# Performance work log

Measured on AMD Instinct MI355X. Metric: run time of the kernel, lower is better.

Reference implementation:

```python
import jax, jax.numpy as jnp
import numpy as np

B, N, K, D, H = 8, 128, 64, 256, 8  # batch, groups, keys-per-query, k_dim (=h_size), n_head


def setup_inputs() -> dict:
    key = jax.random.key(0)
    kq, kk, kv, kw, kb = jax.random.split(key, 5)
    bound = 1.0 / np.sqrt(D)  # torch nn.Bilinear default init bound
    return {
        "q": jax.random.normal(kq, (B, N, 1, D), jnp.float32),
        "k": jax.random.normal(kk, (B, N, K, D), jnp.float32),
        "v": jax.random.normal(kv, (B, N, K, D), jnp.float32),
        "W": jax.random.uniform(kw, (H, D, D), jnp.float32, -bound, bound),
        "b": jax.random.uniform(kb, (H,), jnp.float32, -bound, bound),
    }


def reference(q, k, v, W, b):
    Bs, Ns, Ks, Ds = k.shape
    Hh = W.shape[0]
    qe = q[:, :, 0, :]  # (B,N,D); torch expands q over K, einsum broadcasts instead
    # nn.Bilinear: scores[b,n,k,h] = q[b,n,:] @ W[h] @ k[b,n,k,:] + b[h]
    scores = jnp.einsum('bnd,hde,bnke->bnkh', qe, W, k) + b  # (B,N,K,H)
    # Faithful to torch's .view(B, N, -1, K): row-major reinterpretation of the
    # trailing (K, H) pair as (H, K) — a dim-mixing reshape, not a transpose.
    attn = scores.reshape(Bs, Ns, Hh, Ks)
    attn = jax.nn.softmax(attn, axis=-1)  # softmax over last dim (dropout p=0)
    # matmul(attn, v) -> (B,N,H,Dv); then sum over the head axis
    output = jnp.einsum('bnhk,bnkd->bnd', attn, v)
    return output, attn
```

## Files before the change

kernel.cpp:

```cpp
#include <hip/hip_runtime.h>
#include <math.h>

namespace {

constexpr int D = 256;
constexpr int H = 8;

typedef __attribute__((ext_vector_type(8))) short bf16x8;
typedef __attribute__((ext_vector_type(4))) float f32x4;

__device__ inline unsigned short bf16rn(float x) {
  unsigned u = __builtin_bit_cast(unsigned, x);
  u += 0x7fffu + ((u >> 16) & 1u);
  return (unsigned short)(u >> 16);
}
__device__ inline float bf16tof(unsigned short b) {
  return __builtin_bit_cast(float, (unsigned)b << 16);
}

constexpr size_t OFF_QW  = 0;
constexpr size_t OFF_WFH = (size_t)8 << 20;
constexpr size_t OFF_WFL = (size_t)9 << 20;
constexpr size_t OFF_QFH = (size_t)10 << 20;
constexpr size_t OFF_QFL = ((size_t)10 << 20) + ((size_t)512 << 10);

__global__ __launch_bounds__(256) void prep_kernel(
    const float* __restrict__ q, const float* __restrict__ W,
    char* __restrict__ ws) {
  const int gid = blockIdx.x * 256 + threadIdx.x;
  float e[8];
  char *hi_base, *lo_base;
  size_t outoff;
  if (gid < 65536) {
    const int l = gid & 63, ks = (gid >> 6) & 7, he = gid >> 9;
    const int h = he >> 4, et = he & 15;
    const int d0 = ks * 32 + ((l >> 4) << 3);
    const int ecol = et * 16 + (l & 15);
    const float* src = W + (size_t)h * 65536 + (size_t)d0 * 256 + ecol;
    #pragma unroll
    for (int j = 0; j < 8; ++j) e[j] = src[j * 256];
    hi_base = ws + OFF_WFH; lo_base = ws + OFF_WFL;
    outoff = (size_t)gid * 16;
  } else {
    const int t = gid - 65536;
    const int l = t & 63, ks = (t >> 6) & 7, bt = t >> 9;
    const int row = bt * 16 + (l & 15);
    const int d0 = ks * 32 + ((l >> 4) << 3);
    const float4* src = reinterpret_cast<const float4*>(q + (size_t)row * 256 + d0);
    float4 a = src[0], b = src[1];
    e[0] = a.x; e[1] = a.y; e[2] = a.z; e[3] = a.w;
    e[4] = b.x; e[5] = b.y; e[6] = b.z; e[7] = b.w;
    hi_base = ws + OFF_QFH; lo_base = ws + OFF_QFL;
    outoff = (size_t)t * 16;
  }
  unsigned hw[4], lw[4];
  #pragma unroll
  for (int p = 0; p < 4; ++p) {
    unsigned short h0 = bf16rn(e[2 * p]), h1 = bf16rn(e[2 * p + 1]);
    unsigned short l0 = bf16rn(e[2 * p] - bf16tof(h0));
    unsigned short l1 = bf16rn(e[2 * p + 1] - bf16tof(h1));
    hw[p] = (unsigned)h0 | ((unsigned)h1 << 16);
    lw[p] = (unsigned)l0 | ((unsigned)l1 << 16);
  }
  *reinterpret_cast<uint4*>(hi_base + outoff) = make_uint4(hw[0], hw[1], hw[2], hw[3]);
  *reinterpret_cast<uint4*>(lo_base + outoff) = make_uint4(lw[0], lw[1], lw[2], lw[3]);
}

__global__ __launch_bounds__(256) void qw_mfma_kernel(
    const char* __restrict__ ws_in, float* __restrict__ qW) {
  const int tid = threadIdx.x;
  const int w   = blockIdx.x * 4 + (tid >> 6);
  const int l   = tid & 63;
  const int bng = w >> 5;
  const int heg = w & 31;
  const char* qfh = ws_in + OFF_QFH;
  const char* qfl = ws_in + OFF_QFL;
  const char* wfh = ws_in + OFF_WFH;
  const char* wfl = ws_in + OFF_WFL;

  f32x4 acc[2][4];
  #pragma unroll
  for (int i = 0; i < 2; ++i)
    #pragma unroll
    for (int j = 0; j < 4; ++j) acc[i][j] = {0.f, 0.f, 0.f, 0.f};

  #pragma unroll 2
  for (int ks = 0; ks < 8; ++ks) {
    bf16x8 aH[2], aL[2], bH[4], bL[4];
    #pragma unroll
    for (int i = 0; i < 2; ++i) {
      const size_t off = ((size_t)((bng * 2 + i) * 8 + ks) * 64 + l) * 16;
      aH[i] = *reinterpret_cast<const bf16x8*>(qfh + off);
      aL[i] = *reinterpret_cast<const bf16x8*>(qfl + off);
    }
    #pragma unroll
    for (int j = 0; j < 4; ++j) {
      const size_t off = ((size_t)((heg * 4 + j) * 8 + ks) * 64 + l) * 16;
      bH[j] = *reinterpret_cast<const bf16x8*>(wfh + off);
      bL[j] = *reinterpret_cast<const bf16x8*>(wfl + off);
    }
    #pragma unroll
    for (int i = 0; i < 2; ++i)
      #pragma unroll
      for (int j = 0; j < 4; ++j) {
        acc[i][j] = __builtin_amdgcn_mfma_f32_16x16x32_bf16(aH[i], bH[j], acc[i][j], 0, 0, 0);
        acc[i][j] = __builtin_amdgcn_mfma_f32_16x16x32_bf16(aH[i], bL[j], acc[i][j], 0, 0, 0);
        acc[i][j] = __builtin_amdgcn_mfma_f32_16x16x32_bf16(aL[i], bH[j], acc[i][j], 0, 0, 0);
      }
  }

  const int rbase = (l >> 4) * 4;
  const int col   = l & 15;
  #pragma unroll
  for (int i = 0; i < 2; ++i)
    #pragma unroll
    for (int j = 0; j < 4; ++j) {
      const size_t cidx = (size_t)(heg * 4 + j) * 16 + col;
      #pragma unroll
      for (int r = 0; r < 4; ++r) {
        const int bn = (bng * 2 + i) * 16 + rbase + r;
        qW[(size_t)bn * 2048 + cidx] = acc[i][j][r];
      }
    }
}

constexpr int FA_HI = 0;
constexpr int FB_HI = 16640;
constexpr int WSP_OFF = 24960;
constexpr int SMEM2 = 25472;

__global__ __launch_bounds__(256, 4) void attn_fused_kernel(
    const float* __restrict__ qW, const float* __restrict__ kin,
    const float* __restrict__ vin, const float* __restrict__ bin,
    float* __restrict__ out, float* __restrict__ attn_out) {
  __shared__ alignas(16) long long smem_ll[SMEM2 / 8];
  char* sm = reinterpret_cast<char*>(smem_ll);
  float* wsp = reinterpret_cast<float*>(sm + WSP_OFF);
  const int tid = threadIdx.x;
  const int bn  = blockIdx.x;
  const int wid = tid >> 6;
  const int ln  = tid & 63;

  const float4* k4  = reinterpret_cast<const float4*>(kin) + (size_t)bn * 4096;
  const float4* v4  = reinterpret_cast<const float4*>(vin) + (size_t)bn * 4096;
  const float4* qw4 = reinterpret_cast<const float4*>(qW) + (size_t)bn * 512;
  const float bias = bin[ln & 7];

  float4 kv1[8];
  #pragma unroll
  for (int i = 0; i < 8; ++i) kv1[i] = k4[tid + 256 * i];
  float4 qv0 = qw4[tid];
  float4 qv1 = qw4[tid + 256];

  {
    const int ks = tid >> 5, slot = 32 + (tid & 31);
    *reinterpret_cast<uint4*>(sm + FB_HI + ks * 1040 + slot * 16) =
        make_uint4(0u, 0u, 0u, 0u);
  }

  auto convert_k = [&](const float4* kv) {
    #pragma unroll
    for (int i = 0; i < 8; ++i) {
      int quad = tid + 256 * i;
      int row = quad >> 6, equad = quad & 63;
      int tile = row >> 4, lrow = row & 15;
      int ks = equad >> 3, g = (equad >> 1) & 3, j0 = (equad & 1) * 4;
      int base = tile * 8320 + ks * 1040 + (lrow * 4 + g) * 16 + j0 * 2;
      unsigned short h0 = bf16rn(kv[i].x), h1 = bf16rn(kv[i].y),
                     h2 = bf16rn(kv[i].z), h3 = bf16rn(kv[i].w);
      uint2 hw = make_uint2((unsigned)h0 | ((unsigned)h1 << 16),
                            (unsigned)h2 | ((unsigned)h3 << 16));
      *reinterpret_cast<uint2*>(sm + FA_HI + base) = hw;
    }
  };

  convert_k(kv1);
  #pragma unroll
  for (int i = 0; i < 2; ++i) {
    int p = tid + 256 * i;
    int hh = p >> 6, equad = p & 63;
    int ks = equad >> 3, g = (equad >> 1) & 3, j0 = (equad & 1) * 4;
    int base = ks * 1040 + (hh * 4 + g) * 16 + j0 * 2;
    float4 qv = i == 0 ? qv0 : qv1;
    unsigned short h0 = bf16rn(qv.x), h1 = bf16rn(qv.y),
                   h2 = bf16rn(qv.z), h3 = bf16rn(qv.w);
    uint2 hw = make_uint2((unsigned)h0 | ((unsigned)h1 << 16),
                          (unsigned)h2 | ((unsigned)h3 << 16));
    *reinterpret_cast<uint2*>(sm + FB_HI + base) = hw;
  }

  float4 kv2[8];
  #pragma unroll
  for (int i = 0; i < 8; ++i) kv2[i] = k4[2048 + tid + 256 * i];
  __builtin_amdgcn_sched_barrier(0);
  __syncthreads();

  auto do_phase = [&](int kh, bool first) {
    const int T = wid;
    const int slot_r = (ln & 15) * 4 + (ln >> 4);
    const char* paH = sm + FA_HI + T * 8320 + slot_r * 16;
    const char* pbH = sm + FB_HI + slot_r * 16;
    f32x4 acc = {0.f, 0.f, 0.f, 0.f};
    #pragma unroll
    for (int ks = 0; ks < 8; ++ks) {
      bf16x8 aH = *reinterpret_cast<const bf16x8*>(paH + ks * 1040);
      bf16x8 bH = *reinterpret_cast<const bf16x8*>(pbH + ks * 1040);
      acc = __builtin_amdgcn_mfma_f32_16x16x32_bf16(aH, bH, acc, 0, 0, 0);
    }
    const int col = ln & 15;
    const bool valid = col < 8;
    float x0 = acc[0] + bias, x1 = acc[1] + bias, x2 = acc[2] + bias, x3 = acc[3] + bias;
    float m = valid ? fmaxf(fmaxf(x0, x1), fmaxf(x2, x3)) : -1e30f;
    m = fmaxf(m, __shfl_xor(m, 1, 64));
    m = fmaxf(m, __shfl_xor(m, 2, 64));
    m = fmaxf(m, __shfl_xor(m, 4, 64));
    m = fmaxf(m, __shfl_xor(m, 16, 64));
    float e0 = valid ? expf(x0 - m) : 0.f;
    float e1 = valid ? expf(x1 - m) : 0.f;
    float e2 = valid ? expf(x2 - m) : 0.f;
    float e3 = valid ? expf(x3 - m) : 0.f;
    float s = e0 + e1 + e2 + e3;
    s += __shfl_xor(s, 1, 64);
    s += __shfl_xor(s, 2, 64);
    s += __shfl_xor(s, 4, 64);
    s += __shfl_xor(s, 16, 64);
    float inv = 1.f / s;
    float p0 = e0 * inv, p1 = e1 * inv, p2 = e2 * inv, p3 = e3 * inv;
    if (valid) {
      size_t base = (size_t)bn * 512 + (size_t)(kh * 32 + T * 16 + (ln >> 4) * 4) * 8 + col;
      attn_out[base]      = p0;
      attn_out[base + 8]  = p1;
      attn_out[base + 16] = p2;
      attn_out[base + 24] = p3;
    }
    p0 += __shfl_xor(p0, 32, 64);
    p1 += __shfl_xor(p1, 32, 64);
    p2 += __shfl_xor(p2, 32, 64);
    p3 += __shfl_xor(p3, 32, 64);
    if (ln < 32 && (ln & 15) < 8) {
      const int rb = (ln >> 4) * 4;
      const int c8 = ln & 7;
      float* w = wsp + T * 64;
      if (first) {
        w[(rb + 0) * 8 + c8] = p0;
        w[(rb + 1) * 8 + c8] = p1;
        w[(rb + 2) * 8 + c8] = p2;
        w[(rb + 3) * 8 + c8] = p3;
      } else {
        w[(rb + 0) * 8 + c8] += p0;
        w[(rb + 1) * 8 + c8] += p1;
        w[(rb + 2) * 8 + c8] += p2;
        w[(rb + 3) * 8 + c8] += p3;
      }
    }
  };

  if (wid < 2) do_phase(0, true);
  __syncthreads();

  convert_k(kv2);
  float4 vv[16];
  #pragma unroll
  for (int i = 0; i < 16; ++i) vv[i] = v4[(wid + 4 * i) * 64 + ln];
  __builtin_amdgcn_sched_barrier(0);
  __syncthreads();

  if (wid < 2) do_phase(1, false);
  __syncthreads();

  float4 acc = make_float4(0.f, 0.f, 0.f, 0.f);
  #pragma unroll
  for (int i = 0; i < 16; ++i) {
    const int r = wid + 4 * i;
    float w = wsp[r] + wsp[64 + r];
    acc.x += w * vv[i].x; acc.y += w * vv[i].y;
    acc.z += w * vv[i].z; acc.w += w * vv[i].w;
  }
  float* s_red = reinterpret_cast<float*>(sm);
  *reinterpret_cast<float4*>(&s_red[wid * 260 + (ln << 2)]) = acc;
  __syncthreads();

  out[(size_t)bn * D + tid] =
      s_red[tid] + s_red[260 + tid] + s_red[520 + tid] + s_red[780 + tid];
}

}

extern "C" void kernel_launch(void* const* d_in, const int* in_sizes, int n_in,
                              void* d_out, int out_size, void* d_ws, size_t ws_size,
                              hipStream_t stream) {
  const float* q = (const float*)d_in[0];
  const float* k = (const float*)d_in[1];
  const float* v = (const float*)d_in[2];
  const float* W = (const float*)d_in[3];
  const float* b = (const float*)d_in[4];

  float* out  = (float*)d_out;
  float* attn = out + 262144;
  char*  ws   = (char*)d_ws;
  float* qWbuf = (float*)(ws + OFF_QW);

  hipLaunchKernelGGL(prep_kernel,       dim3(384),  dim3(256), 0, stream, q, W, ws);
  hipLaunchKernelGGL(qw_mfma_kernel,    dim3(256),  dim3(256), 0, stream, ws, qWbuf);
  hipLaunchKernelGGL(attn_fused_kernel, dim3(1024), dim3(256), 0, stream,
                     qWbuf, k, v, b, out, attn);
}
```

Measured before the change: 43.53 us.

## Load K directly into MFMA registers and use all four waves for scores

Each wave now loads its 16 K rows from global memory straight into registers in MFMA A-operand layout and converts them to bf16 in registers, which removes the LDS staging of K and its two-phase schedule. All four waves compute scores and softmax in one pass instead of two waves over two phases, and per-wave weights are summed in the V reduction. V loads move after the softmax barrier and are issued inline, so they no longer overlap the score computation. LDS use drops substantially, which may allow higher occupancy, but global K loads are now strided per lane.

```diff
diff --git a/kernel.cpp b/kernel.cpp
--- a/kernel.cpp
+++ b/kernel.cpp
@@ -124,160 +124,122 @@
     }
 }
 
-constexpr int FA_HI = 0;
-constexpr int FB_HI = 16640;
-constexpr int WSP_OFF = 24960;
-constexpr int SMEM2 = 25472;
+constexpr int FB2   = 0;
+constexpr int WSP2  = 8320;
+constexpr int SMEM3 = 9344;
 
 __global__ __launch_bounds__(256, 4) void attn_fused_kernel(
     const float* __restrict__ qW, const float* __restrict__ kin,
     const float* __restrict__ vin, const float* __restrict__ bin,
     float* __restrict__ out, float* __restrict__ attn_out) {
-  __shared__ alignas(16) long long smem_ll[SMEM2 / 8];
+  __shared__ alignas(16) long long smem_ll[SMEM3 / 8];
   char* sm = reinterpret_cast<char*>(smem_ll);
-  float* wsp = reinterpret_cast<float*>(sm + WSP_OFF);
+  float* wsp = reinterpret_cast<float*>(sm + WSP2);
   const int tid = threadIdx.x;
   const int bn  = blockIdx.x;
   const int wid = tid >> 6;
   const int ln  = tid & 63;
 
-  const float4* k4  = reinterpret_cast<const float4*>(kin) + (size_t)bn * 4096;
-  const float4* v4  = reinterpret_cast<const float4*>(vin) + (size_t)bn * 4096;
+  const float* arow = kin + (size_t)bn * 16384 +
+                      (size_t)(wid * 16 + (ln & 15)) * 256 + ((ln >> 4) << 3);
+  float4 ka[16];
+  #pragma unroll
+  for (int ks = 0; ks < 8; ++ks) {
+    ka[2 * ks]     = *reinterpret_cast<const float4*>(arow + ks * 32);
+    ka[2 * ks + 1] = *reinterpret_cast<const float4*>(arow + ks * 32 + 4);
+  }
   const float4* qw4 = reinterpret_cast<const float4*>(qW) + (size_t)bn * 512;
-  const float bias = bin[ln & 7];
-
-  float4 kv1[8];
-  #pragma unroll
-  for (int i = 0; i < 8; ++i) kv1[i] = k4[tid + 256 * i];
   float4 qv0 = qw4[tid];
   float4 qv1 = qw4[tid + 256];
 
   {
     const int ks = tid >> 5, slot = 32 + (tid & 31);
-    *reinterpret_cast<uint4*>(sm + FB_HI + ks * 1040 + slot * 16) =
+    *reinterpret_cast<uint4*>(sm + FB2 + ks * 1040 + slot * 16) =
         make_uint4(0u, 0u, 0u, 0u);
   }
-
-  auto convert_k = [&](const float4* kv) {
-    #pragma unroll
-    for (int i = 0; i < 8; ++i) {
-      int quad = tid + 256 * i;
-      int row = quad >> 6, equad = quad & 63;
-      int tile = row >> 4, lrow = row & 15;
-      int ks = equad >> 3, g = (equad >> 1) & 3, j0 = (equad & 1) * 4;
-      int base = tile * 8320 + ks * 1040 + (lrow * 4 + g) * 16 + j0 * 2;
-      unsigned short h0 = bf16rn(kv[i].x), h1 = bf16rn(kv[i].y),
-                     h2 = bf16rn(kv[i].z), h3 = bf16rn(kv[i].w);
-      uint2 hw = make_uint2((unsigned)h0 | ((unsigned)h1 << 16),
-                            (unsigned)h2 | ((unsigned)h3 << 16));
-      *reinterpret_cast<uint2*>(sm + FA_HI + base) = hw;
-    }
-  };
-
-  convert_k(kv1);
   #pragma unroll
   for (int i = 0; i < 2; ++i) {
     int p = tid + 256 * i;
     int hh = p >> 6, equad = p & 63;
     int ks = equad >> 3, g = (equad >> 1) & 3, j0 = (equad & 1) * 4;
-    int base = ks * 1040 + (hh * 4 + g) * 16 + j0 * 2;
+    int base = FB2 + ks * 1040 + (hh * 4 + g) * 16 + j0 * 2;
     float4 qv = i == 0 ? qv0 : qv1;
     unsigned short h0 = bf16rn(qv.x), h1 = bf16rn(qv.y),
                    h2 = bf16rn(qv.z), h3 = bf16rn(qv.w);
-    uint2 hw = make_uint2((unsigned)h0 | ((unsigned)h1 << 16),
-                          (unsigned)h2 | ((unsigned)h3 << 16));
-    *reinterpret_cast<uint2*>(sm + FB_HI + base) = hw;
-  }
-
-  float4 kv2[8];
-  #pragma unroll
-  for (int i = 0; i < 8; ++i) kv2[i] = k4[2048 + tid + 256 * i];
-  __builtin_amdgcn_sched_barrier(0);
+    *reinterpret_cast<uint2*>(sm + base) =
+        make_uint2((unsigned)h0 | ((unsigned)h1 << 16),
+                   (unsigned)h2 | ((unsigned)h3 << 16));
+  }
   __syncthreads();
 
-  auto do_phase = [&](int kh, bool first) {
-    const int T = wid;
-    const int slot_r = (ln & 15) * 4 + (ln >> 4);
-    const char* paH = sm + FA_HI + T * 8320 + slot_r * 16;
-    const char* pbH = sm + FB_HI + slot_r * 16;
-    f32x4 acc = {0.f, 0.f, 0.f, 0.f};
-    #pragma unroll
-    for (int ks = 0; ks < 8; ++ks) {
-      bf16x8 aH = *reinterpret_cast<const bf16x8*>(paH + ks * 1040);
-      bf16x8 bH = *reinterpret_cast<const bf16x8*>(pbH + ks * 1040);
-      acc = __builtin_amdgcn_mfma_f32_16x16x32_bf16(aH, bH, acc, 0, 0, 0);
-    }
-    const int col = ln & 15;
-    const bool valid = col < 8;
-    float x0 = acc[0] + bias, x1 = acc[1] + bias, x2 = acc[2] + bias, x3 = acc[3] + bias;
-    float m = valid ? fmaxf(fmaxf(x0, x1), fmaxf(x2, x3)) : -1e30f;
-    m = fmaxf(m, __shfl_xor(m, 1, 64));
-    m = fmaxf(m, __shfl_xor(m, 2, 64));
-    m = fmaxf(m, __shfl_xor(m, 4, 64));
-    m = fmaxf(m, __shfl_xor(m, 16, 64));
-    float e0 = valid ? expf(x0 - m) : 0.f;
-    float e1 = valid ? expf(x1 - m) : 0.f;
-    float e2 = valid ? expf(x2 - m) : 0.f;
-    float e3 = valid ? expf(x3 - m) : 0.f;
-    float s = e0 + e1 + e2 + e3;
-    s += __shfl_xor(s, 1, 64);
-    s += __shfl_xor(s, 2, 64);
-    s += __shfl_xor(s, 4, 64);
-    s += __shfl_xor(s, 16, 64);
-    float inv = 1.f / s;
-    float p0 = e0 * inv, p1 = e1 * inv, p2 = e2 * inv, p3 = e3 * inv;
-    if (valid) {
-      size_t base = (size_t)bn * 512 + (size_t)(kh * 32 + T * 16 + (ln >> 4) * 4) * 8 + col;
-      attn_out[base]      = p0;
-      attn_out[base + 8]  = p1;
-      attn_out[base + 16] = p2;
-      attn_out[base + 24] = p3;
-    }
-    p0 += __shfl_xor(p0, 32, 64);
-    p1 += __shfl_xor(p1, 32, 64);
-    p2 += __shfl_xor(p2, 32, 64);
-    p3 += __shfl_xor(p3, 32, 64);
-    if (ln < 32 && (ln & 15) < 8) {
-      const int rb = (ln >> 4) * 4;
-      const int c8 = ln & 7;
-      float* w = wsp + T * 64;
-      if (first) {
-        w[(rb + 0) * 8 + c8] = p0;
-        w[(rb + 1) * 8 + c8] = p1;
-        w[(rb + 2) * 8 + c8] = p2;
-        w[(rb + 3) * 8 + c8] = p3;
-      } else {
-        w[(rb + 0) * 8 + c8] += p0;
-        w[(rb + 1) * 8 + c8] += p1;
-        w[(rb + 2) * 8 + c8] += p2;
-        w[(rb + 3) * 8 + c8] += p3;
-      }
-    }
-  };
-
-  if (wid < 2) do_phase(0, true);
+  const int slot_r = (ln & 15) * 4 + (ln >> 4);
+  const char* pbH = sm + FB2 + slot_r * 16;
+  f32x4 acc = {0.f, 0.f, 0.f, 0.f};
+  #pragma unroll
+  for (int ks = 0; ks < 8; ++ks) {
+    const float4 a0 = ka[2 * ks], a1 = ka[2 * ks + 1];
+    bf16x8 aH;
+    aH[0] = (short)bf16rn(a0.x); aH[1] = (short)bf16rn(a0.y);
+    aH[2] = (short)bf16rn(a0.z); aH[3] = (short)bf16rn(a0.w);
+    aH[4] = (short)bf16rn(a1.x); aH[5] = (short)bf16rn(a1.y);
+    aH[6] = (short)bf16rn(a1.z); aH[7] = (short)bf16rn(a1.w);
+    bf16x8 bH = *reinterpret_cast<const bf16x8*>(pbH + ks * 1040);
+    acc = __builtin_amdgcn_mfma_f32_16x16x32_bf16(aH, bH, acc, 0, 0, 0);
+  }
+
+  const float bias = bin[ln & 7];
+  const int col = ln & 15;
+  const bool valid = col < 8;
+  float x0 = acc[0] + bias, x1 = acc[1] + bias, x2 = acc[2] + bias, x3 = acc[3] + bias;
+  float m = valid ? fmaxf(fmaxf(x0, x1), fmaxf(x2, x3)) : -1e30f;
+  m = fmaxf(m, __shfl_xor(m, 1, 64));
+  m = fmaxf(m, __shfl_xor(m, 2, 64));
+  m = fmaxf(m, __shfl_xor(m, 4, 64));
+  m = fmaxf(m, __shfl_xor(m, 16, 64));
+  float e0 = valid ? expf(x0 - m) : 0.f;
+  float e1 = valid ? expf(x1 - m) : 0.f;
+  float e2 = valid ? expf(x2 - m) : 0.f;
+  float e3 = valid ? expf(x3 - m) : 0.f;
+  float s = e0 + e1 + e2 + e3;
+  s += __shfl_xor(s, 1, 64);
+  s += __shfl_xor(s, 2, 64);
+  s += __shfl_xor(s, 4, 64);
+  s += __shfl_xor(s, 16, 64);
+  float inv = 1.f / s;
+  float p0 = e0 * inv, p1 = e1 * inv, p2 = e2 * inv, p3 = e3 * inv;
+  if (valid) {
+    size_t base = (size_t)bn * 512 + (size_t)(wid * 16 + (ln >> 4) * 4) * 8 + col;
+    attn_out[base]      = p0;
+    attn_out[base + 8]  = p1;
+    attn_out[base + 16] = p2;
+    attn_out[base + 24] = p3;
+  }
+  p0 += __shfl_xor(p0, 32, 64);
+  p1 += __shfl_xor(p1, 32, 64);
+  p2 += __shfl_xor(p2, 32, 64);
+  p3 += __shfl_xor(p3, 32, 64);
+  if (ln < 32 && (ln & 15) < 8) {
+    const int rb = (ln >> 4) * 4;
+    const int c8 = ln & 7;
+    float* w = wsp + wid * 64;
+    w[(rb + 0) * 8 + c8] = p0;
+    w[(rb + 1) * 8 + c8] = p1;
+    w[(rb + 2) * 8 + c8] = p2;
+    w[(rb + 3) * 8 + c8] = p3;
+  }
   __syncthreads();
 
-  convert_k(kv2);
-  float4 vv[16];
-  #pragma unroll
-  for (int i = 0; i < 16; ++i) vv[i] = v4[(wid + 4 * i) * 64 + ln];
-  __builtin_amdgcn_sched_barrier(0);
-  __syncthreads();
-
-  if (wid < 2) do_phase(1, false);
-  __syncthreads();
-
-  float4 acc = make_float4(0.f, 0.f, 0.f, 0.f);
+  const float4* v4 = reinterpret_cast<const float4*>(vin) + (size_t)bn * 4096;
+  float4 av = make_float4(0.f, 0.f, 0.f, 0.f);
   #pragma unroll
   for (int i = 0; i < 16; ++i) {
     const int r = wid + 4 * i;
-    float w = wsp[r] + wsp[64 + r];
-    acc.x += w * vv[i].x; acc.y += w * vv[i].y;
-    acc.z += w * vv[i].z; acc.w += w * vv[i].w;
+    float w = wsp[r] + wsp[64 + r] + wsp[128 + r] + wsp[192 + r];
+    float4 vv = v4[r * 64 + ln];
+    av.x += w * vv.x; av.y += w * vv.y; av.z += w * vv.z; av.w += w * vv.w;
   }
   float* s_red = reinterpret_cast<float*>(sm);
-  *reinterpret_cast<float4*>(&s_red[wid * 260 + (ln << 2)]) = acc;
+  *reinterpret_cast<float4*>(&s_red[wid * 260 + (ln << 2)]) = av;
   __syncthreads();
 
   out[(size_t)bn * D + tid] =
```

Measured after the change: 42.24 us. -3.0%, faster.
